# Optimization experiments

Measured on AMD Instinct MI355X. Metric: run time of the kernel, lower is better.

Reference implementation:

```python
import jax, jax.numpy as jnp
import numpy as np

B, N, E = 128, 4096, 262144  # batch, num_vertices, num_edges


def setup_inputs() -> dict:
    key = jax.random.key(0)
    k1, k2, k3, k4, k5 = jax.random.split(key, 5)
    x = jax.random.normal(k1, (B, N), dtype=jnp.float32)
    error = jax.random.normal(k2, (B, N), dtype=jnp.float32)
    w = jax.random.normal(k3, (N, N), dtype=jnp.float32) * 0.02  # dense weight matrix, masked by adj in orig
    src = jax.random.randint(k4, (E,), 0, N)
    tgt = jax.random.randint(k5, (E,), 0, N)
    edge_index = jnp.stack([src, tgt]).astype(jnp.int32)  # [2, E]
    return {"x": x, "error": error, "w": w, "edge_index": edge_index}


def reference(x, error, w, edge_index):
    # Activation f = tanh, dfdx = 1 - tanh^2 (set_activation convention).
    src, tgt = edge_index[0], edge_index[1]
    w_e = w[src, tgt]  # per-edge weight gather, [E]

    # --- PredictionMessagePassing (flow='target_to_source', aggr='add') ---
    # message: f(x_j) * weight with x_j = x[tgt]; aggregated at src nodes.
    fx_t = jnp.tanh(x[:, tgt])                          # [B, E]
    mu = jnp.zeros_like(x).at[:, src].add(fx_t * w_e)   # scatter-add -> [B, N]

    # --- GradientMessagePassing (flow='source_to_target', aggr='add') ---
    # message: dfdx(x_i) * error_j * weight with x_i = x[tgt], error_j = error[src];
    # aggregated at tgt nodes; update: error - aggr_out.
    dfdx_t = 1.0 - fx_t * fx_t                          # [B, E]
    aggr = jnp.zeros_like(x).at[:, tgt].add(dfdx_t * error[:, src] * w_e)
    dEdx = error - aggr                                 # [B, N]

    return mu, dEdx
```

## Files before the change

kernel.cpp:

```cpp
#include <hip/hip_runtime.h>
#include <hip/hip_fp16.h>
#include <math.h>

#define B    128
#define NV   4096
#define NE   262144
#define CAP  192
#define KSC  128
#define EPB  2048
#define NS   8192
#define SCOLS 64


__device__ inline float2 h2f(unsigned u) {
    __half2 h;
    *reinterpret_cast<unsigned*>(&h) = u;
    return __half22float2(h);
}
__device__ inline __half2 u2h2(unsigned u) {
    __half2 h;
    *reinterpret_cast<unsigned*>(&h) = u;
    return h;
}

__global__ __launch_bounds__(256)
void k_tc(const float* __restrict__ x, const float* __restrict__ err,
          const int* __restrict__ ei,
          ushort* __restrict__ Th, ushort* __restrict__ Eh,
          unsigned* __restrict__ hist) {
    __shared__ unsigned shm[NS];
    const int t = threadIdx.x, blk = blockIdx.x;

    if (blk < 512) {
        float* tile0 = (float*)shm;
        float* tile1 = tile0 + 1056;
        const int n0 = (blk & 127) * 32;
        const int b0 = (blk >> 7) * 32;
        const int a = t & 31, c0 = t >> 5;
#pragma unroll
        for (int r = 0; r < 4; ++r) {
            int c = c0 + 8 * r;
            int gi = (b0 + c) * NV + (n0 + a);
            tile0[c * 33 + a] = tanhf(x[gi]);
            tile1[c * 33 + a] = err[gi];
        }
        __syncthreads();
#pragma unroll
        for (int r = 0; r < 4; ++r) {
            int c = c0 + 8 * r;
            int go = (n0 + c) * B + (b0 + a);
            Th[go] = __half_as_ushort(__float2half_rn(tile0[a * 33 + c]));
            Eh[go] = __half_as_ushort(__float2half_rn(tile1[a * 33 + c]));
        }
    } else {
        const int blk2 = blk - 512;
#pragma unroll
        for (int i = 0; i < NS / 256; ++i) shm[t + 256 * i] = 0u;
        __syncthreads();
        const int base = blk2 * EPB + t;
#pragma unroll
        for (int i = 0; i < 8; ++i) {
            const int e = base + 256 * i;
            atomicAdd(&shm[ei[e]], 1u);
            atomicAdd(&shm[4096 + ei[NE + e]], 1u);
        }
        __syncthreads();
        unsigned* hrow = hist + (size_t)blk2 * NS;
#pragma unroll
        for (int i = 0; i < NS / 256; ++i) hrow[t + 256 * i] = shm[t + 256 * i];
    }
}

__global__ __launch_bounds__(256)
void k_scan(const unsigned* __restrict__ hist, unsigned* __restrict__ off,
            unsigned* __restrict__ count) {
    __shared__ unsigned p[KSC * SCOLS];
    const int t  = threadIdx.x;
    const int n0 = blockIdx.x * SCOLS;
#pragma unroll
    for (int i = 0; i < (KSC * SCOLS) / 256; ++i) {
        int l = t + 256 * i;
        p[l] = hist[(size_t)(l >> 6) * NS + n0 + (l & 63)];
    }
    __syncthreads();
    const int col = t >> 2, seg = t & 3;
    unsigned s = 0;
#pragma unroll
    for (int j = 0; j < KSC / 4; ++j) s += p[(seg * (KSC / 4) + j) * SCOLS + col];
    unsigned inc = s;
    unsigned v1 = __shfl_up(inc, 1, 4); if (seg >= 1) inc += v1;
    unsigned v2 = __shfl_up(inc, 2, 4); if (seg >= 2) inc += v2;
    unsigned run = inc - s;
    if (seg == 3) count[n0 + col] = inc;
#pragma unroll
    for (int j = 0; j < KSC / 4; ++j) {
        int idx = (seg * (KSC / 4) + j) * SCOLS + col;
        unsigned old = p[idx];
        p[idx] = run;
        run += old;
    }
    __syncthreads();
#pragma unroll
    for (int i = 0; i < (KSC * SCOLS) / 256; ++i) {
        int l = t + 256 * i;
        off[(size_t)(l >> 6) * NS + n0 + (l & 63)] = p[l];
    }
}

__global__ __launch_bounds__(256)
void k_place(const int* __restrict__ ei, const float* __restrict__ w,
             const unsigned* __restrict__ off,
             unsigned* __restrict__ es, unsigned* __restrict__ et) {
    __shared__ unsigned slot[NS];
    const int t = threadIdx.x, blk = blockIdx.x;
    const unsigned* orow = off + (size_t)blk * NS;
#pragma unroll
    for (int i = 0; i < NS / 256; ++i) slot[t + 256 * i] = orow[t + 256 * i];
    const int base = blk * EPB + t;
    int sn[8], tn[8];
    unsigned wh[8];
#pragma unroll
    for (int i = 0; i < 8; ++i) {
        const int e = base + 256 * i;
        sn[i] = ei[e];
        tn[i] = ei[NE + e];
    }
#pragma unroll
    for (int i = 0; i < 8; ++i)
        wh[i] = (unsigned)__half_as_ushort(
            __float2half_rn(w[(size_t)sn[i] * NV + tn[i]]));
    __syncthreads();
    unsigned pp[8], qq[8];
#pragma unroll
    for (int i = 0; i < 8; ++i) {
        pp[i] = atomicAdd(&slot[sn[i]], 1u);
        qq[i] = atomicAdd(&slot[4096 + tn[i]], 1u);
    }
#pragma unroll
    for (int i = 0; i < 8; ++i) {
        if (pp[i] < CAP) es[sn[i] * CAP + pp[i]] = ((unsigned)tn[i] << 16) | wh[i];
        if (qq[i] < CAP) et[tn[i] * CAP + qq[i]] = ((unsigned)sn[i] << 16) | wh[i];
    }
}

__global__ __launch_bounds__(64)
void k_proc(const unsigned* __restrict__ count,
            const unsigned* __restrict__ es, const unsigned* __restrict__ et,
            const unsigned* __restrict__ Th2, const unsigned* __restrict__ Eh2,
            float* __restrict__ out) {
    const int raw    = blockIdx.x;
    const bool is_mu = raw < NV;
    const int b2     = is_mu ? raw : raw - NV;
    const int node   = (b2 & 7) * (NV / 8) + (b2 >> 3);
    int n_e = (int)count[is_mu ? node : NV + node];
    if (n_e > CAP) n_e = CAP;
    const unsigned* ed  = (is_mu ? es : et) + node * CAP;
    const int4*     ed4 = (const int4*)ed;
    const unsigned* srcH = is_mu ? Th2 : Eh2;
    const int lane = threadIdx.x;

    __half2 a0 = u2h2(0u), a1 = u2h2(0u), a2 = u2h2(0u), a3 = u2h2(0u);
    __half2 a4 = u2h2(0u), a5 = u2h2(0u), a6 = u2h2(0u), a7 = u2h2(0u);
    int k = 0;
    for (; k + 8 <= n_e; k += 8) {
        int4 mA = ed4[(k >> 2) + 0];
        int4 mB = ed4[(k >> 2) + 1];
        const unsigned r0 = (unsigned)mA.x, r1 = (unsigned)mA.y;
        const unsigned r2 = (unsigned)mA.z, r3 = (unsigned)mA.w;
        const unsigned r4 = (unsigned)mB.x, r5 = (unsigned)mB.y;
        const unsigned r6 = (unsigned)mB.z, r7 = (unsigned)mB.w;
        unsigned g0 = srcH[(r0 >> 16) * (B / 2) + lane];
        unsigned g1 = srcH[(r1 >> 16) * (B / 2) + lane];
        unsigned g2 = srcH[(r2 >> 16) * (B / 2) + lane];
        unsigned g3 = srcH[(r3 >> 16) * (B / 2) + lane];
        unsigned g4 = srcH[(r4 >> 16) * (B / 2) + lane];
        unsigned g5 = srcH[(r5 >> 16) * (B / 2) + lane];
        unsigned g6 = srcH[(r6 >> 16) * (B / 2) + lane];
        unsigned g7 = srcH[(r7 >> 16) * (B / 2) + lane];
        __half2 w0 = u2h2(__builtin_amdgcn_perm(r0, r0, 0x01000100u));
        __half2 w1 = u2h2(__builtin_amdgcn_perm(r1, r1, 0x01000100u));
        __half2 w2 = u2h2(__builtin_amdgcn_perm(r2, r2, 0x01000100u));
        __half2 w3 = u2h2(__builtin_amdgcn_perm(r3, r3, 0x01000100u));
        __half2 w4 = u2h2(__builtin_amdgcn_perm(r4, r4, 0x01000100u));
        __half2 w5 = u2h2(__builtin_amdgcn_perm(r5, r5, 0x01000100u));
        __half2 w6 = u2h2(__builtin_amdgcn_perm(r6, r6, 0x01000100u));
        __half2 w7 = u2h2(__builtin_amdgcn_perm(r7, r7, 0x01000100u));
        a0 = __hfma2(u2h2(g0), w0, a0);
        a1 = __hfma2(u2h2(g1), w1, a1);
        a2 = __hfma2(u2h2(g2), w2, a2);
        a3 = __hfma2(u2h2(g3), w3, a3);
        a4 = __hfma2(u2h2(g4), w4, a4);
        a5 = __hfma2(u2h2(g5), w5, a5);
        a6 = __hfma2(u2h2(g6), w6, a6);
        a7 = __hfma2(u2h2(g7), w7, a7);
    }
    for (; k < n_e; ++k) {
        unsigned r = ed[k];
        unsigned g = srcH[(r >> 16) * (B / 2) + lane];
        a0 = __hfma2(u2h2(g), u2h2(__builtin_amdgcn_perm(r, r, 0x01000100u)), a0);
    }
    float2 f0 = __half22float2(a0), f1 = __half22float2(a1);
    float2 f2 = __half22float2(a2), f3 = __half22float2(a3);
    float2 f4 = __half22float2(a4), f5 = __half22float2(a5);
    float2 f6 = __half22float2(a6), f7 = __half22float2(a7);
    f0.x += f1.x; f0.y += f1.y;  f2.x += f3.x; f2.y += f3.y;
    f4.x += f5.x; f4.y += f5.y;  f6.x += f7.x; f6.y += f7.y;
    f0.x += f2.x; f0.y += f2.y;  f4.x += f6.x; f4.y += f6.y;
    float2 acc = make_float2(f0.x + f4.x, f0.y + f4.y);

    const int b0 = 2 * lane;
    if (is_mu) {
        out[(size_t)b0 * NV + node]       = acc.x;
        out[(size_t)(b0 + 1) * NV + node] = acc.y;
    } else {
        const int oi = node * (B / 2) + lane;
        float2 th = h2f(Th2[oi]);
        float2 er = h2f(Eh2[oi]);
        float* o2 = out + (size_t)B * NV;
        o2[(size_t)b0 * NV + node]       = er.x - (1.f - th.x * th.x) * acc.x;
        o2[(size_t)(b0 + 1) * NV + node] = er.y - (1.f - th.y * th.y) * acc.y;
    }
}

extern "C" void kernel_launch(void* const* d_in, const int* in_sizes, int n_in,
                              void* d_out, int out_size, void* d_ws, size_t ws_size,
                              hipStream_t stream) {
    const float* x   = (const float*)d_in[0];
    const float* err = (const float*)d_in[1];
    const float* w   = (const float*)d_in[2];
    const int*   ei  = (const int*)d_in[3];
    float* out = (float*)d_out;

    const int NB = NV * B;
    ushort*   Th    = (ushort*)d_ws;
    ushort*   Eh    = Th + NB;
    unsigned* hist  = (unsigned*)(Eh + NB);
    unsigned* off   = hist + (size_t)KSC * NS;
    unsigned* count = off + (size_t)KSC * NS;
    unsigned* es    = count + NS;
    unsigned* et    = es + (size_t)NV * CAP;

    k_tc<<<512 + KSC, 256, 0, stream>>>(x, err, ei, Th, Eh, hist);
    k_scan<<<NS / SCOLS, 256, 0, stream>>>(hist, off, count);
    k_place<<<KSC, 256, 0, stream>>>(ei, w, off, es, et);
    k_proc<<<2 * NV, 64, 0, stream>>>(count, es, et,
                                      (const unsigned*)Th, (const unsigned*)Eh, out);
}
```

Baseline: 133.6 us.

## Move weight gather into histogram kernel and fuse scan with transpose

The pipeline changes from transpose+hist / scan / place to hist+weight-gather / transpose+scan / place. The random weight gather from the dense matrix now runs in the small histogram kernel and is stored as a compact half-precision array, so k_place only does a coalesced read. The scan now shares a launch with the tanh/error transpose, which hides the scan's latency behind that work. The cost is an extra workspace array and a histogram kernel that runs on only 128 blocks while also carrying the scattered gather latency.

```diff
diff --git a/kernel.cpp b/kernel.cpp
--- a/kernel.cpp
+++ b/kernel.cpp
@@ -24,10 +24,44 @@
 }
 
 __global__ __launch_bounds__(256)
-void k_tc(const float* __restrict__ x, const float* __restrict__ err,
-          const int* __restrict__ ei,
+void k_hist(const int* __restrict__ ei, const float* __restrict__ w,
+            unsigned* __restrict__ hist, ushort* __restrict__ wst) {
+    __shared__ unsigned shm[NS];
+    const int t = threadIdx.x, blk = blockIdx.x;
+#pragma unroll
+    for (int i = 0; i < NS / 256; ++i) shm[t + 256 * i] = 0u;
+    __syncthreads();
+    const int base = blk * EPB + t;
+    int sn[8], tn[8];
+#pragma unroll
+    for (int i = 0; i < 8; ++i) {
+        const int e = base + 256 * i;
+        sn[i] = ei[e];
+        tn[i] = ei[NE + e];
+    }
+    ushort wh[8];
+#pragma unroll
+    for (int i = 0; i < 8; ++i)
+        wh[i] = __half_as_ushort(__float2half_rn(w[(size_t)sn[i] * NV + tn[i]]));
+#pragma unroll
+    for (int i = 0; i < 8; ++i) {
+        atomicAdd(&shm[sn[i]], 1u);
+        atomicAdd(&shm[4096 + tn[i]], 1u);
+    }
+#pragma unroll
+    for (int i = 0; i < 8; ++i)
+        wst[base + 256 * i] = wh[i];
+    __syncthreads();
+    unsigned* hrow = hist + (size_t)blk * NS;
+#pragma unroll
+    for (int i = 0; i < NS / 256; ++i) hrow[t + 256 * i] = shm[t + 256 * i];
+}
+
+__global__ __launch_bounds__(256)
+void k_ts(const float* __restrict__ x, const float* __restrict__ err,
           ushort* __restrict__ Th, ushort* __restrict__ Eh,
-          unsigned* __restrict__ hist) {
+          const unsigned* __restrict__ hist, unsigned* __restrict__ off,
+          unsigned* __restrict__ count) {
     __shared__ unsigned shm[NS];
     const int t = threadIdx.x, blk = blockIdx.x;
 
@@ -53,62 +87,41 @@
             Eh[go] = __half_as_ushort(__float2half_rn(tile1[a * 33 + c]));
         }
     } else {
-        const int blk2 = blk - 512;
-#pragma unroll
-        for (int i = 0; i < NS / 256; ++i) shm[t + 256 * i] = 0u;
+        unsigned* p = shm;
+        const int n0 = (blk - 512) * SCOLS;
+#pragma unroll
+        for (int i = 0; i < (KSC * SCOLS) / 256; ++i) {
+            int l = t + 256 * i;
+            p[l] = hist[(size_t)(l >> 6) * NS + n0 + (l & 63)];
+        }
         __syncthreads();
-        const int base = blk2 * EPB + t;
-#pragma unroll
-        for (int i = 0; i < 8; ++i) {
-            const int e = base + 256 * i;
-            atomicAdd(&shm[ei[e]], 1u);
-            atomicAdd(&shm[4096 + ei[NE + e]], 1u);
+        const int col = t >> 2, seg = t & 3;
+        unsigned s = 0;
+#pragma unroll
+        for (int j = 0; j < KSC / 4; ++j) s += p[(seg * (KSC / 4) + j) * SCOLS + col];
+        unsigned inc = s;
+        unsigned v1 = __shfl_up(inc, 1, 4); if (seg >= 1) inc += v1;
+        unsigned v2 = __shfl_up(inc, 2, 4); if (seg >= 2) inc += v2;
+        unsigned run = inc - s;
+        if (seg == 3) count[n0 + col] = inc;
+#pragma unroll
+        for (int j = 0; j < KSC / 4; ++j) {
+            int idx = (seg * (KSC / 4) + j) * SCOLS + col;
+            unsigned old = p[idx];
+            p[idx] = run;
+            run += old;
         }
         __syncthreads();
-        unsigned* hrow = hist + (size_t)blk2 * NS;
-#pragma unroll
-        for (int i = 0; i < NS / 256; ++i) hrow[t + 256 * i] = shm[t + 256 * i];
+#pragma unroll
+        for (int i = 0; i < (KSC * SCOLS) / 256; ++i) {
+            int l = t + 256 * i;
+            off[(size_t)(l >> 6) * NS + n0 + (l & 63)] = p[l];
+        }
     }
 }
 
 __global__ __launch_bounds__(256)
-void k_scan(const unsigned* __restrict__ hist, unsigned* __restrict__ off,
-            unsigned* __restrict__ count) {
-    __shared__ unsigned p[KSC * SCOLS];
-    const int t  = threadIdx.x;
-    const int n0 = blockIdx.x * SCOLS;
-#pragma unroll
-    for (int i = 0; i < (KSC * SCOLS) / 256; ++i) {
-        int l = t + 256 * i;
-        p[l] = hist[(size_t)(l >> 6) * NS + n0 + (l & 63)];
-    }
-    __syncthreads();
-    const int col = t >> 2, seg = t & 3;
-    unsigned s = 0;
-#pragma unroll
-    for (int j = 0; j < KSC / 4; ++j) s += p[(seg * (KSC / 4) + j) * SCOLS + col];
-    unsigned inc = s;
-    unsigned v1 = __shfl_up(inc, 1, 4); if (seg >= 1) inc += v1;
-    unsigned v2 = __shfl_up(inc, 2, 4); if (seg >= 2) inc += v2;
-    unsigned run = inc - s;
-    if (seg == 3) count[n0 + col] = inc;
-#pragma unroll
-    for (int j = 0; j < KSC / 4; ++j) {
-        int idx = (seg * (KSC / 4) + j) * SCOLS + col;
-        unsigned old = p[idx];
-        p[idx] = run;
-        run += old;
-    }
-    __syncthreads();
-#pragma unroll
-    for (int i = 0; i < (KSC * SCOLS) / 256; ++i) {
-        int l = t + 256 * i;
-        off[(size_t)(l >> 6) * NS + n0 + (l & 63)] = p[l];
-    }
-}
-
-__global__ __launch_bounds__(256)
-void k_place(const int* __restrict__ ei, const float* __restrict__ w,
+void k_place(const int* __restrict__ ei, const ushort* __restrict__ wst,
              const unsigned* __restrict__ off,
              unsigned* __restrict__ es, unsigned* __restrict__ et) {
     __shared__ unsigned slot[NS];
@@ -124,11 +137,8 @@
         const int e = base + 256 * i;
         sn[i] = ei[e];
         tn[i] = ei[NE + e];
-    }
-#pragma unroll
-    for (int i = 0; i < 8; ++i)
-        wh[i] = (unsigned)__half_as_ushort(
-            __float2half_rn(w[(size_t)sn[i] * NV + tn[i]]));
+        wh[i] = (unsigned)wst[e];
+    }
     __syncthreads();
     unsigned pp[8], qq[8];
 #pragma unroll
@@ -234,15 +244,16 @@
     const int NB = NV * B;
     ushort*   Th    = (ushort*)d_ws;
     ushort*   Eh    = Th + NB;
-    unsigned* hist  = (unsigned*)(Eh + NB);
+    ushort*   wst   = Eh + NB;
+    unsigned* hist  = (unsigned*)(wst + NE);
     unsigned* off   = hist + (size_t)KSC * NS;
     unsigned* count = off + (size_t)KSC * NS;
     unsigned* es    = count + NS;
     unsigned* et    = es + (size_t)NV * CAP;
 
-    k_tc<<<512 + KSC, 256, 0, stream>>>(x, err, ei, Th, Eh, hist);
-    k_scan<<<NS / SCOLS, 256, 0, stream>>>(hist, off, count);
-    k_place<<<KSC, 256, 0, stream>>>(ei, w, off, es, et);
+    k_hist<<<KSC, 256, 0, stream>>>(ei, w, hist, wst);
+    k_ts<<<512 + KSC, 256, 0, stream>>>(x, err, Th, Eh, hist, off, count);
+    k_place<<<KSC, 256, 0, stream>>>(ei, wst, off, es, et);
     k_proc<<<2 * NV, 64, 0, stream>>>(count, es, et,
                                       (const unsigned*)Th, (const unsigned*)Eh, out);
 }
```

After: 133.1 us. About the same (-0.4%).
